# Kernel optimization log

Hardware: AMD Instinct MI355X
Metric: run time of the kernel (lower is better)

## Reference

```python
import jax, jax.numpy as jnp
import numpy as np

H = 1024
F = 4096  # base_ffn_dim = hidden * 4
WIDTHS = [256, 512]  # adapters; idx 2 -> width==hidden -> identity
EPS = 1e-5


def _xavier(key, fan_in, fan_out, gain):
    a = gain * np.sqrt(6.0 / (fan_in + fan_out))
    return jax.random.uniform(key, (fan_in, fan_out), jnp.float32, -a, a)


def _layernorm(x, g, b):
    mu = jnp.mean(x, axis=-1, keepdims=True)
    var = jnp.var(x, axis=-1, keepdims=True)
    return (x - mu) * jax.lax.rsqrt(var + EPS) * g + b


def setup_inputs() -> dict:
    key = jax.random.key(0)
    ks = jax.random.split(key, 12)
    g = 1.0 / np.sqrt(2.0)
    B, S = 4, 2048
    return {
        "x": jax.random.normal(ks[0], (B, S, H), jnp.float32),
        "width_multiplier": jax.random.uniform(ks[1], (B, S, 1), jnp.float32),
        "width_idx": jax.random.randint(ks[2], (B, S), 0, 3, jnp.int32),
        "ln_in_g": jnp.ones((H,), jnp.float32),
        "ln_in_b": jnp.zeros((H,), jnp.float32),
        "W1": _xavier(ks[3], H, F, g),
        "b1": jnp.zeros((F,), jnp.float32),
        "ln_h_g": jnp.ones((F,), jnp.float32),
        "ln_h_b": jnp.zeros((F,), jnp.float32),
        "W2": _xavier(ks[4], F, H, g),
        "b2": jnp.zeros((H,), jnp.float32),
        "a256_w1": _xavier(ks[5], H, 256, g),
        "a256_b1": jnp.zeros((256,), jnp.float32),
        "a256_w2": _xavier(ks[6], 256, H, g),
        "a256_b2": jnp.zeros((H,), jnp.float32),
        "a512_w1": _xavier(ks[7], H, 512, g),
        "a512_b1": jnp.zeros((512,), jnp.float32),
        "a512_w2": _xavier(ks[8], 512, H, g),
        "a512_b2": jnp.zeros((H,), jnp.float32),
    }


def reference(x, width_multiplier, width_idx,
              ln_in_g, ln_in_b, W1, b1, ln_h_g, ln_h_b, W2, b2,
              a256_w1, a256_b1, a256_w2, a256_b2,
              a512_w1, a512_b1, a512_w2, a512_b2):
    gelu = lambda t: jax.nn.gelu(t, approximate=False)  # torch nn.GELU exact
    x_norm = _layernorm(x, ln_in_g, ln_in_b)
    # base FFN path
    h = gelu(jnp.einsum("bsh,hf->bsf", x_norm, W1) + b1)
    h = _layernorm(h, ln_h_g, ln_h_b)
    base = jnp.einsum("bsf,fh->bsh", h, W2) + b2
    # width adapters (routed per token by width_idx)
    ad0 = jnp.einsum("bsw,wh->bsh", gelu(jnp.einsum("bsh,hw->bsw", x_norm, a256_w1) + a256_b1), a256_w2) + a256_b2
    ad1 = jnp.einsum("bsw,wh->bsh", gelu(jnp.einsum("bsh,hw->bsw", x_norm, a512_w1) + a512_b1), a512_w2) + a512_b2
    idx = width_idx[..., None]
    adaptive = jnp.where(idx == 0, ad0, jnp.where(idx == 1, ad1, x_norm))
    return base * width_multiplier + adaptive * (1.0 - width_multiplier)
```

## Files before the change

kernel.cpp:

```cpp
#include <hip/hip_runtime.h>
#include <cstdint>
#include <cstddef>

typedef unsigned short u16x8 __attribute__((ext_vector_type(8)));
typedef unsigned short u16x4 __attribute__((ext_vector_type(4)));
typedef __bf16 bf16x8 __attribute__((ext_vector_type(8)));
typedef float f32x4 __attribute__((ext_vector_type(4)));

__device__ __forceinline__ float b2f(unsigned short u) {
    union { unsigned int i; float f; } v;
    v.i = ((unsigned int)u) << 16;
    return v.f;
}

__device__ __forceinline__ unsigned short f2b(float f) {
    union { float f; unsigned int i; } v;
    v.f = f;
    unsigned int x = v.i;
    unsigned int lsb = (x >> 16) & 1u;
    x += 0x7FFFu + lsb;
    return (unsigned short)(x >> 16);
}

__device__ __forceinline__ float gelu_exact(float x) {
    return 0.5f * x * (1.0f + erff(x * 0.70710678118654752f));
}

__device__ __forceinline__ void ld_lds16(const unsigned short* g, unsigned short* l) {
    __builtin_amdgcn_global_load_lds(
        (const __attribute__((address_space(1))) void*)g,
        (__attribute__((address_space(3))) void*)l, 16, 0, 0);
}

__global__ void transpose_f32_bf16(const float* __restrict__ in,
                                   unsigned short* __restrict__ out, int R, int C,
                                   const float* __restrict__ scale) {
    __shared__ float tile[32][33];
    int x = blockIdx.x * 32 + threadIdx.x;
    int y0 = blockIdx.y * 32;
    for (int k = 0; k < 32; k += 8)
        tile[threadIdx.y + k][threadIdx.x] = in[(size_t)(y0 + threadIdx.y + k) * C + x];
    __syncthreads();
    int ox = y0 + threadIdx.x;
    int oy = blockIdx.x * 32;
    float sc = scale ? scale[ox] : 1.0f;
    for (int k = 0; k < 32; k += 8)
        out[(size_t)(oy + threadIdx.y + k) * R + ox] = f2b(tile[threadIdx.x][threadIdx.y + k] * sc);
}

__global__ void concat_bias(const float* __restrict__ b0, const float* __restrict__ b1,
                            float* __restrict__ out) {
    int t = threadIdx.x + blockIdx.x * blockDim.x;
    if (t < 256) out[t] = b0[t];
    else if (t < 768) out[t] = b1[t - 256];
}

__global__ void init_c01(const float* __restrict__ b2, float* __restrict__ c0b2,
                         float* __restrict__ c1) {
    int n = blockIdx.x * 256 + threadIdx.x;
    c0b2[n] = b2[n];
    c1[n] = 0.0f;
}

__global__ void prep_c01(const float* __restrict__ W2, const float* __restrict__ g,
                         const float* __restrict__ b, float* __restrict__ c0b2,
                         float* __restrict__ c1, int K, int N) {
    int n = blockIdx.x * 256 + threadIdx.x;
    int k0 = blockIdx.y * 256;
    float p0 = 0.f, p1 = 0.f;
    for (int k = k0; k < k0 + 256; ++k) {
        float w = W2[(size_t)k * N + n];
        p0 += b[k] * w;
        p1 += g[k] * w;
    }
    atomicAdd(&c0b2[n], p0);
    atomicAdd(&c1[n], p1);
}

__global__ __launch_bounds__(256) void rowstats4096(const unsigned short* __restrict__ h,
                                                    float* __restrict__ st) {
    const int row = blockIdx.x;
    const int t = threadIdx.x;
    const u16x8* p = (const u16x8*)(h + (size_t)row * 4096);
    float s = 0.f, s2 = 0.f;
#pragma unroll
    for (int i = 0; i < 2; ++i) {
        u16x8 v = p[t + (i << 8)];
#pragma unroll
        for (int r = 0; r < 8; ++r) { float f = b2f(v[r]); s += f; s2 += f * f; }
    }
#pragma unroll
    for (int o = 32; o > 0; o >>= 1) {
        s  += __shfl_down(s, o, 64);
        s2 += __shfl_down(s2, o, 64);
    }
    __shared__ float red[8];
    int lane = t & 63, w = t >> 6;
    if (lane == 0) { red[w] = s; red[4 + w] = s2; }
    __syncthreads();
    if (t == 0) {
        float ss = red[0] + red[1] + red[2] + red[3];
        float qq = red[4] + red[5] + red[6] + red[7];
        const float inv = 1.0f / 4096.0f;
        float mu = ss * inv;
        float var = qq * inv - mu * mu;
        float rs = rsqrtf(var + 1e-5f);
        st[2 * (size_t)row]     = rs;
        st[2 * (size_t)row + 1] = rs * mu;
    }
}

__global__ __launch_bounds__(256) void ln1024(const float* __restrict__ in,
                                              unsigned short* __restrict__ out,
                                              const float* __restrict__ g,
                                              const float* __restrict__ b) {
    const int row = blockIdx.x;
    const int t = threadIdx.x;
    f32x4 v = ((const f32x4*)(in + (size_t)row * 1024))[t];
    float s = v[0] + v[1] + v[2] + v[3];
    float s2 = v[0] * v[0] + v[1] * v[1] + v[2] * v[2] + v[3] * v[3];
#pragma unroll
    for (int o = 32; o > 0; o >>= 1) {
        s  += __shfl_down(s, o, 64);
        s2 += __shfl_down(s2, o, 64);
    }
    __shared__ float red[8];
    int lane = t & 63, w = t >> 6;
    if (lane == 0) { red[w] = s; red[4 + w] = s2; }
    __syncthreads();
    if (t == 0) {
        red[0] = red[0] + red[1] + red[2] + red[3];
        red[4] = red[4] + red[5] + red[6] + red[7];
    }
    __syncthreads();
    const float inv_n = 1.0f / 1024.0f;
    float mu = red[0] * inv_n;
    float var = red[4] * inv_n - mu * mu;
    float rs = rsqrtf(var + 1e-5f);
    f32x4 gv = ((const f32x4*)g)[t];
    f32x4 bv = ((const f32x4*)b)[t];
    u16x4 ov;
#pragma unroll
    for (int r = 0; r < 4; ++r) ov[r] = f2b((v[r] - mu) * rs * gv[r] + bv[r]);
    ((u16x4*)(out + (size_t)row * 1024))[t] = ov;
}

template <int EPI>
__global__ __launch_bounds__(256) void gemm_bt(
    const unsigned short* __restrict__ A, int lda,
    const unsigned short* __restrict__ BT, int ldb,
    const float* __restrict__ bias, unsigned short* __restrict__ Cb,
    float* __restrict__ Cf, int M, int N, int K,
    const int* __restrict__ idx, int match,
    const float* __restrict__ wm,
    const unsigned short* __restrict__ adaptive,
    const unsigned short* __restrict__ xn,
    const float* __restrict__ c1v,
    const float* __restrict__ rstat) {
    __shared__ __align__(16) unsigned short As[2][128 * 32];
    __shared__ __align__(16) unsigned short Bs[2][128 * 32];

    const int t = threadIdx.x;

    int id = blockIdx.y * gridDim.x + blockIdx.x;
    const int nwg = gridDim.x * gridDim.y;
    if ((nwg & 7) == 0) {
        const int cpx = nwg >> 3;
        id = (id & 7) * cpx + (id >> 3);
    }
    const int bx = id % gridDim.x;
    const int by = id / gridDim.x;
    const int m0 = by * 128;
    const int n0 = bx * 128;

    const int lane = t & 63;
    const int wid = t >> 6;

    const int srow = lane >> 2;
    const int sch  = (lane & 3) ^ (srow & 3);
    const int scol = sch << 3;

    const int wr = (wid >> 1) << 6;
    const int wc = (wid & 1) << 6;
    const int ml = lane & 15;
    const int q = lane >> 4;
    const int qsw = ((q ^ (ml & 3)) << 3);

    f32x4 acc[4][4];
#pragma unroll
    for (int i = 0; i < 4; ++i)
#pragma unroll
        for (int j = 0; j < 4; ++j)
#pragma unroll
            for (int r = 0; r < 4; ++r) acc[i][j][r] = 0.0f;

    const int nk = K >> 5;

#define STAGE(KT, BUF)                                                          \
    {                                                                           \
        _Pragma("unroll")                                                       \
        for (int hh = 0; hh < 2; ++hh) {                                        \
            int rbase = wid * 32 + hh * 16;                                     \
            int row = rbase + srow;                                             \
            ld_lds16(A  + (size_t)(m0 + row) * lda + (KT) * 32 + scol,          \
                     &As[BUF][rbase * 32]);                                     \
            ld_lds16(BT + (size_t)(n0 + row) * ldb + (KT) * 32 + scol,          \
                     &Bs[BUF][rbase * 32]);                                     \
        }                                                                       \
    }

    STAGE(0, 0);
    for (int kt = 0; kt < nk; ++kt) {
        const int cur = kt & 1;
        __syncthreads();
        if (kt + 1 < nk) STAGE(kt + 1, cur ^ 1);

        bf16x8 af[4], bf[4];
#pragma unroll
        for (int i = 0; i < 4; ++i)
            af[i] = *(const bf16x8*)(&As[cur][(wr + i * 16 + ml) * 32 + qsw]);
#pragma unroll
        for (int j = 0; j < 4; ++j)
            bf[j] = *(const bf16x8*)(&Bs[cur][(wc + j * 16 + ml) * 32 + qsw]);
#pragma unroll
        for (int i = 0; i < 4; ++i)
#pragma unroll
            for (int j = 0; j < 4; ++j)
                acc[i][j] = __builtin_amdgcn_mfma_f32_16x16x32_bf16(af[i], bf[j], acc[i][j], 0, 0, 0);
    }
#undef STAGE

#pragma unroll
    for (int i = 0; i < 4; ++i) {
        float rsv[4], rmv[4], wv[4];
        int idv[4];
        if (EPI == 1 || EPI == 2) {
#pragma unroll
            for (int r = 0; r < 4; ++r) {
                int row = m0 + wr + i * 16 + q * 4 + r;
                idv[r] = idx[row];
                if (EPI == 2) {
                    wv[r] = wm[row];
                    rsv[r] = rstat[2 * (size_t)row];
                    rmv[r] = rstat[2 * (size_t)row + 1];
                }
            }
        }
#pragma unroll
        for (int j = 0; j < 4; ++j) {
            int col = n0 + wc + j * 16 + ml;
            float bv = bias[col];
            float c1c = (EPI == 2) ? c1v[col] : 0.0f;
#pragma unroll
            for (int r = 0; r < 4; ++r) {
                int row = m0 + wr + i * 16 + q * 4 + r;
                size_t off = (size_t)row * N + col;
                if (EPI == 0) {
                    Cb[off] = f2b(gelu_exact(acc[i][j][r] + bv));
                } else if (EPI == 1) {
                    if (idv[r] == match) Cb[off] = f2b(acc[i][j][r] + bv);
                } else {
                    float bval = rsv[r] * acc[i][j][r] + bv - rmv[r] * c1c;
                    float a = b2f((idv[r] <= 1) ? adaptive[off] : xn[off]);
                    Cf[off] = bval * wv[r] + a * (1.0f - wv[r]);
                }
            }
        }
    }
}

extern "C" void kernel_launch(void* const* d_in, const int* in_sizes, int n_in,
                              void* d_out, int out_size, void* d_ws, size_t ws_size,
                              hipStream_t stream) {
    const float* x       = (const float*)d_in[0];
    const float* wm      = (const float*)d_in[1];
    const int*   widx    = (const int*)d_in[2];
    const float* ln_in_g = (const float*)d_in[3];
    const float* ln_in_b = (const float*)d_in[4];
    const float* W1      = (const float*)d_in[5];
    const float* b1      = (const float*)d_in[6];
    const float* ln_h_g  = (const float*)d_in[7];
    const float* ln_h_b  = (const float*)d_in[8];
    const float* W2      = (const float*)d_in[9];
    const float* b2      = (const float*)d_in[10];
    const float* a256_w1 = (const float*)d_in[11];
    const float* a256_b1 = (const float*)d_in[12];
    const float* a256_w2 = (const float*)d_in[13];
    const float* a256_b2 = (const float*)d_in[14];
    const float* a512_w1 = (const float*)d_in[15];
    const float* a512_b1 = (const float*)d_in[16];
    const float* a512_w2 = (const float*)d_in[17];
    const float* a512_b2 = (const float*)d_in[18];
    float* out = (float*)d_out;

    const int T = 8192, H = 1024, F = 4096;

    unsigned short* ws0   = (unsigned short*)d_ws;
    unsigned short* xn    = ws0;
    unsigned short* h     = xn    + (size_t)T * H;
    unsigned short* tt    = h     + (size_t)T * F;
    unsigned short* adp   = tt    + (size_t)T * 768;
    unsigned short* W1T   = adp   + (size_t)T * H;
    unsigned short* W2T   = W1T   + (size_t)H * F;
    unsigned short* awup  = W2T   + (size_t)F * H;
    unsigned short* aw2T0 = awup  + (size_t)768 * H;
    unsigned short* aw2T1 = aw2T0 + (size_t)H * 256;
    float*          ab1   = (float*)(aw2T1 + (size_t)H * 512);
    float*          stats = ab1 + 768;
    float*          c0b2  = stats + (size_t)T * 2;
    float*          c1    = c0b2 + H;

    dim3 tb(32, 8);
    init_c01<<<H / 256, 256, 0, stream>>>(b2, c0b2, c1);
    prep_c01<<<dim3(H / 256, F / 256), 256, 0, stream>>>(W2, ln_h_g, ln_h_b, c0b2, c1, F, H);

    transpose_f32_bf16<<<dim3(F / 32,   H / 32), tb, 0, stream>>>(W1, W1T, H, F, nullptr);
    transpose_f32_bf16<<<dim3(H / 32,   F / 32), tb, 0, stream>>>(W2, W2T, F, H, ln_h_g);
    transpose_f32_bf16<<<dim3(256 / 32, H / 32), tb, 0, stream>>>(a256_w1, awup, H, 256, nullptr);
    transpose_f32_bf16<<<dim3(512 / 32, H / 32), tb, 0, stream>>>(a512_w1, awup + (size_t)256 * H, H, 512, nullptr);
    transpose_f32_bf16<<<dim3(H / 32, 256 / 32), tb, 0, stream>>>(a256_w2, aw2T0, 256, H, nullptr);
    transpose_f32_bf16<<<dim3(H / 32, 512 / 32), tb, 0, stream>>>(a512_w2, aw2T1, 512, H, nullptr);
    concat_bias<<<3, 256, 0, stream>>>(a256_b1, a512_b1, ab1);

    ln1024<<<T, 256, 0, stream>>>(x, xn, ln_in_g, ln_in_b);

    gemm_bt<0><<<dim3(F / 128, T / 128), 256, 0, stream>>>(
        xn, H, W1T, H, b1, h, nullptr, T, F, H, nullptr, 0, nullptr, nullptr, nullptr, nullptr, nullptr);

    rowstats4096<<<T, 256, 0, stream>>>(h, stats);

    gemm_bt<0><<<dim3(768 / 128, T / 128), 256, 0, stream>>>(
        xn, H, awup, H, ab1, tt, nullptr, T, 768, H, nullptr, 0, nullptr, nullptr, nullptr, nullptr, nullptr);

    gemm_bt<1><<<dim3(H / 128, T / 128), 256, 0, stream>>>(
        tt, 768, aw2T0, 256, a256_b2, adp, nullptr, T, H, 256, widx, 0, nullptr, nullptr, nullptr, nullptr, nullptr);
    gemm_bt<1><<<dim3(H / 128, T / 128), 256, 0, stream>>>(
        tt + 256, 768, aw2T1, 512, a512_b2, adp, nullptr, T, H, 512, widx, 1, nullptr, nullptr, nullptr, nullptr, nullptr);

    gemm_bt<2><<<dim3(H / 128, T / 128), 256, 0, stream>>>(
        h, F, W2T, F, c0b2, nullptr, out, T, H, F, widx, 0, wm, adp, xn, c1, stats);
}
```

Measured before the change: 460.6 us.

## Add 256x256-tile 8-wave GEMM with grid swizzle for the W1 up-projection

Replaces the 128x128 generic GEMM used for the first FFN GEMM (8192x4096x1024) with a dedicated 256x256 tile kernel. It uses 512 threads, BK=64 double-buffered LDS loads, XOR-swizzled LDS layout, s_setprio around MFMA clusters and an XCD-aware block remap. The larger tile raises arithmetic intensity and cuts global traffic per FLOP. In exchange it uses 128KB of LDS per block, which limits occupancy, and the grid shrinks to 512 blocks, which risks wave-quantization tail effects across CUs.

```diff
diff --git a/kernel.cpp b/kernel.cpp
--- a/kernel.cpp
+++ b/kernel.cpp
@@ -143,6 +143,133 @@
 #pragma unroll
     for (int r = 0; r < 4; ++r) ov[r] = f2b((v[r] - mu) * rs * gv[r] + bv[r]);
     ((u16x4*)(out + (size_t)row * 1024))[t] = ov;
+}
+
+__global__ __launch_bounds__(512, 2) void gemm256_gelu(
+    const unsigned short* __restrict__ A, int lda,
+    const unsigned short* __restrict__ BT, int ldb,
+    const float* __restrict__ bias, unsigned short* __restrict__ Cb,
+    int M, int N, int K) {
+    __shared__ __align__(16) unsigned short As[2][256 * 64];
+    __shared__ __align__(16) unsigned short Bs[2][256 * 64];
+
+    const int t = threadIdx.x;
+
+    int id = blockIdx.y * gridDim.x + blockIdx.x;
+    const int nwg = gridDim.x * gridDim.y;
+    {
+        const int cpx = nwg >> 3;
+        id = (id & 7) * cpx + (id >> 3);
+    }
+    const int m0 = (id / gridDim.x) * 256;
+    const int n0 = (id % gridDim.x) * 256;
+
+    const int lane = t & 63;
+    const int wid = t >> 6;
+    const int wmr = (wid >> 2) << 7;
+    const int wnr = (wid & 3) << 6;
+    const int ml = lane & 15;
+    const int q = lane >> 4;
+
+    const int srow8 = lane >> 3;
+    const int scol = (((lane & 7) ^ (srow8 & 7)) << 3);
+
+    const int c0 = ((q ^ (ml & 7)) << 3);
+    const int c1 = c0 ^ 32;
+
+    f32x4 acc[8][4];
+#pragma unroll
+    for (int i = 0; i < 8; ++i)
+#pragma unroll
+        for (int j = 0; j < 4; ++j)
+#pragma unroll
+            for (int r = 0; r < 4; ++r) acc[i][j][r] = 0.0f;
+
+    const int nk = K >> 6;
+
+#define STAGE256(KT, BUF)                                                       \
+    {                                                                           \
+        const unsigned short* asrc =                                            \
+            A + (size_t)(m0 + wid * 8 + srow8) * lda + (KT) * 64 + scol;        \
+        const unsigned short* bsrc =                                            \
+            BT + (size_t)(n0 + wid * 8 + srow8) * ldb + (KT) * 64 + scol;       \
+        _Pragma("unroll")                                                       \
+        for (int s = 0; s < 4; ++s) {                                           \
+            ld_lds16(asrc + (size_t)s * 64 * lda, &As[BUF][(s * 64 + wid * 8) * 64]); \
+            ld_lds16(bsrc + (size_t)s * 64 * ldb, &Bs[BUF][(s * 64 + wid * 8) * 64]); \
+        }                                                                       \
+    }
+
+#define LDA256(QI)                                                              \
+    _Pragma("unroll")                                                           \
+    for (int i2 = 0; i2 < 4; ++i2) {                                            \
+        int row = wmr + (QI) * 64 + i2 * 16 + ml;                               \
+        afq[i2][0] = *(const bf16x8*)(&As[cur][(row << 6) + c0]);               \
+        afq[i2][1] = *(const bf16x8*)(&As[cur][(row << 6) + c1]);               \
+    }
+
+#define LDB256(DST, QJ)                                                         \
+    _Pragma("unroll")                                                           \
+    for (int j2 = 0; j2 < 2; ++j2) {                                            \
+        int row = wnr + (QJ) * 32 + j2 * 16 + ml;                               \
+        DST[j2][0] = *(const bf16x8*)(&Bs[cur][(row << 6) + c0]);               \
+        DST[j2][1] = *(const bf16x8*)(&Bs[cur][(row << 6) + c1]);               \
+    }
+
+#define MFMA16(I0, J0, BF)                                                      \
+    __builtin_amdgcn_s_barrier();                                               \
+    __builtin_amdgcn_s_setprio(1);                                              \
+    _Pragma("unroll")                                                           \
+    for (int i2 = 0; i2 < 4; ++i2)                                              \
+        _Pragma("unroll")                                                       \
+        for (int j2 = 0; j2 < 2; ++j2) {                                        \
+            acc[(I0) + i2][(J0) + j2] = __builtin_amdgcn_mfma_f32_16x16x32_bf16( \
+                afq[i2][0], BF[j2][0], acc[(I0) + i2][(J0) + j2], 0, 0, 0);     \
+            acc[(I0) + i2][(J0) + j2] = __builtin_amdgcn_mfma_f32_16x16x32_bf16( \
+                afq[i2][1], BF[j2][1], acc[(I0) + i2][(J0) + j2], 0, 0, 0);     \
+        }                                                                       \
+    __builtin_amdgcn_s_setprio(0);                                              \
+    __builtin_amdgcn_s_barrier();
+
+    STAGE256(0, 0);
+    for (int kt = 0; kt < nk; ++kt) {
+        const int cur = kt & 1;
+        if (kt + 1 < nk) {
+            STAGE256(kt + 1, cur ^ 1);
+            asm volatile("s_waitcnt vmcnt(8)" ::: "memory");
+        } else {
+            asm volatile("s_waitcnt vmcnt(0)" ::: "memory");
+        }
+        __builtin_amdgcn_s_barrier();
+
+        bf16x8 afq[4][2], b0f[2][2], b1f[2][2];
+        LDA256(0);
+        LDB256(b0f, 0);
+        MFMA16(0, 0, b0f);
+        LDB256(b1f, 1);
+        MFMA16(0, 2, b1f);
+        LDA256(1);
+        MFMA16(4, 2, b1f);
+        MFMA16(4, 0, b0f);
+    }
+#undef STAGE256
+#undef LDA256
+#undef LDB256
+#undef MFMA16
+
+#pragma unroll
+    for (int i = 0; i < 8; ++i) {
+#pragma unroll
+        for (int j = 0; j < 4; ++j) {
+            int col = n0 + wnr + j * 16 + ml;
+            float bv = bias[col];
+#pragma unroll
+            for (int r = 0; r < 4; ++r) {
+                int row = m0 + wmr + i * 16 + q * 4 + r;
+                Cb[(size_t)row * N + col] = f2b(gelu_exact(acc[i][j][r] + bv));
+            }
+        }
+    }
 }
 
 template <int EPI>
@@ -324,8 +451,8 @@
 
     ln1024<<<T, 256, 0, stream>>>(x, xn, ln_in_g, ln_in_b);
 
-    gemm_bt<0><<<dim3(F / 128, T / 128), 256, 0, stream>>>(
-        xn, H, W1T, H, b1, h, nullptr, T, F, H, nullptr, 0, nullptr, nullptr, nullptr, nullptr, nullptr);
+    gemm256_gelu<<<dim3(F / 256, T / 256), 512, 0, stream>>>(
+        xn, H, W1T, H, b1, h, T, F, H);
 
     rowstats4096<<<T, 256, 0, stream>>>(h, stats);
 
```

Result: slower. 471.5 us (+2.4%).

## Merge prep, adapter and stats kernels into fewer horizontally fused launches

Applied to the files above, without the earlier changes.

Combines all weight transposes, bias concat, the c0/c1 precompute and the input layernorm into one block-dispatched prep kernel. The adapter up-projection GEMM now shares a launch with the hidden row statistics, and the two adapter down-projection GEMMs share a single launch, cutting launch count and inter-kernel gaps so independent small work can overlap. The c01 precompute drops atomics in favour of 4 blocks each looping over the full K, which serialises that work into a long tail inside the prep kernel. Larger fused kernels may also have higher register and shared-memory footprints for the simple branches.

```diff
diff --git a/kernel.cpp b/kernel.cpp
--- a/kernel.cpp
+++ b/kernel.cpp
@@ -32,89 +32,50 @@
         (__attribute__((address_space(3))) void*)l, 16, 0, 0);
 }
 
-__global__ void transpose_f32_bf16(const float* __restrict__ in,
-                                   unsigned short* __restrict__ out, int R, int C,
-                                   const float* __restrict__ scale) {
+
+__device__ __forceinline__ void transp_body(const float* __restrict__ in,
+                                            unsigned short* __restrict__ out,
+                                            int R, int C,
+                                            const float* __restrict__ scale,
+                                            int bx, int by) {
     __shared__ float tile[32][33];
-    int x = blockIdx.x * 32 + threadIdx.x;
-    int y0 = blockIdx.y * 32;
+    const int tx = threadIdx.x & 31;
+    const int ty = threadIdx.x >> 5;
+    int x = bx * 32 + tx;
+    int y0 = by * 32;
     for (int k = 0; k < 32; k += 8)
-        tile[threadIdx.y + k][threadIdx.x] = in[(size_t)(y0 + threadIdx.y + k) * C + x];
+        tile[ty + k][tx] = in[(size_t)(y0 + ty + k) * C + x];
     __syncthreads();
-    int ox = y0 + threadIdx.x;
-    int oy = blockIdx.x * 32;
+    int ox = y0 + tx;
+    int oy = bx * 32;
     float sc = scale ? scale[ox] : 1.0f;
     for (int k = 0; k < 32; k += 8)
-        out[(size_t)(oy + threadIdx.y + k) * R + ox] = f2b(tile[threadIdx.x][threadIdx.y + k] * sc);
-}
-
-__global__ void concat_bias(const float* __restrict__ b0, const float* __restrict__ b1,
-                            float* __restrict__ out) {
-    int t = threadIdx.x + blockIdx.x * blockDim.x;
-    if (t < 256) out[t] = b0[t];
-    else if (t < 768) out[t] = b1[t - 256];
-}
-
-__global__ void init_c01(const float* __restrict__ b2, float* __restrict__ c0b2,
-                         float* __restrict__ c1) {
-    int n = blockIdx.x * 256 + threadIdx.x;
-    c0b2[n] = b2[n];
-    c1[n] = 0.0f;
-}
-
-__global__ void prep_c01(const float* __restrict__ W2, const float* __restrict__ g,
-                         const float* __restrict__ b, float* __restrict__ c0b2,
-                         float* __restrict__ c1, int K, int N) {
-    int n = blockIdx.x * 256 + threadIdx.x;
-    int k0 = blockIdx.y * 256;
+        out[(size_t)(oy + ty + k) * R + ox] = f2b(tile[tx][ty + k] * sc);
+}
+
+__device__ __forceinline__ void c01_body(const float* __restrict__ W2,
+                                         const float* __restrict__ g,
+                                         const float* __restrict__ b,
+                                         const float* __restrict__ b2,
+                                         float* __restrict__ c0b2,
+                                         float* __restrict__ c1,
+                                         int K, int N, int blocal) {
+    int n = (blocal << 8) + threadIdx.x;
     float p0 = 0.f, p1 = 0.f;
-    for (int k = k0; k < k0 + 256; ++k) {
+    for (int k = 0; k < K; ++k) {
         float w = W2[(size_t)k * N + n];
         p0 += b[k] * w;
         p1 += g[k] * w;
     }
-    atomicAdd(&c0b2[n], p0);
-    atomicAdd(&c1[n], p1);
-}
-
-__global__ __launch_bounds__(256) void rowstats4096(const unsigned short* __restrict__ h,
-                                                    float* __restrict__ st) {
-    const int row = blockIdx.x;
-    const int t = threadIdx.x;
-    const u16x8* p = (const u16x8*)(h + (size_t)row * 4096);
-    float s = 0.f, s2 = 0.f;
-#pragma unroll
-    for (int i = 0; i < 2; ++i) {
-        u16x8 v = p[t + (i << 8)];
-#pragma unroll
-        for (int r = 0; r < 8; ++r) { float f = b2f(v[r]); s += f; s2 += f * f; }
-    }
-#pragma unroll
-    for (int o = 32; o > 0; o >>= 1) {
-        s  += __shfl_down(s, o, 64);
-        s2 += __shfl_down(s2, o, 64);
-    }
-    __shared__ float red[8];
-    int lane = t & 63, w = t >> 6;
-    if (lane == 0) { red[w] = s; red[4 + w] = s2; }
-    __syncthreads();
-    if (t == 0) {
-        float ss = red[0] + red[1] + red[2] + red[3];
-        float qq = red[4] + red[5] + red[6] + red[7];
-        const float inv = 1.0f / 4096.0f;
-        float mu = ss * inv;
-        float var = qq * inv - mu * mu;
-        float rs = rsqrtf(var + 1e-5f);
-        st[2 * (size_t)row]     = rs;
-        st[2 * (size_t)row + 1] = rs * mu;
-    }
-}
-
-__global__ __launch_bounds__(256) void ln1024(const float* __restrict__ in,
-                                              unsigned short* __restrict__ out,
-                                              const float* __restrict__ g,
-                                              const float* __restrict__ b) {
-    const int row = blockIdx.x;
+    c0b2[n] = p0 + b2[n];
+    c1[n] = p1;
+}
+
+__device__ __forceinline__ void ln1024_body(const float* __restrict__ in,
+                                            unsigned short* __restrict__ out,
+                                            const float* __restrict__ g,
+                                            const float* __restrict__ b,
+                                            int row) {
     const int t = threadIdx.x;
     f32x4 v = ((const f32x4*)(in + (size_t)row * 1024))[t];
     float s = v[0] + v[1] + v[2] + v[3];
@@ -145,31 +106,62 @@
     ((u16x4*)(out + (size_t)row * 1024))[t] = ov;
 }
 
+__device__ __forceinline__ void rowstats_body(const unsigned short* __restrict__ h,
+                                              float* __restrict__ st, int row) {
+    const int t = threadIdx.x;
+    const u16x8* p = (const u16x8*)(h + (size_t)row * 4096);
+    float s = 0.f, s2 = 0.f;
+#pragma unroll
+    for (int i = 0; i < 2; ++i) {
+        u16x8 v = p[t + (i << 8)];
+#pragma unroll
+        for (int r = 0; r < 8; ++r) { float f = b2f(v[r]); s += f; s2 += f * f; }
+    }
+#pragma unroll
+    for (int o = 32; o > 0; o >>= 1) {
+        s  += __shfl_down(s, o, 64);
+        s2 += __shfl_down(s2, o, 64);
+    }
+    __shared__ float red2[8];
+    int lane = t & 63, w = t >> 6;
+    if (lane == 0) { red2[w] = s; red2[4 + w] = s2; }
+    __syncthreads();
+    if (t == 0) {
+        float ss = red2[0] + red2[1] + red2[2] + red2[3];
+        float qq = red2[4] + red2[5] + red2[6] + red2[7];
+        const float inv = 1.0f / 4096.0f;
+        float mu = ss * inv;
+        float var = qq * inv - mu * mu;
+        float rs = rsqrtf(var + 1e-5f);
+        st[2 * (size_t)row]     = rs;
+        st[2 * (size_t)row + 1] = rs * mu;
+    }
+}
+
 template <int EPI>
-__global__ __launch_bounds__(256) void gemm_bt(
+__device__ __forceinline__ void gemm_body(
+    unsigned short (*As)[128 * 32], unsigned short (*Bs)[128 * 32],
+    int fid, int nbx, int nby,
     const unsigned short* __restrict__ A, int lda,
     const unsigned short* __restrict__ BT, int ldb,
     const float* __restrict__ bias, unsigned short* __restrict__ Cb,
-    float* __restrict__ Cf, int M, int N, int K,
+    float* __restrict__ Cf, int N, int K,
     const int* __restrict__ idx, int match,
     const float* __restrict__ wm,
     const unsigned short* __restrict__ adaptive,
     const unsigned short* __restrict__ xn,
     const float* __restrict__ c1v,
     const float* __restrict__ rstat) {
-    __shared__ __align__(16) unsigned short As[2][128 * 32];
-    __shared__ __align__(16) unsigned short Bs[2][128 * 32];
-
     const int t = threadIdx.x;
 
-    int id = blockIdx.y * gridDim.x + blockIdx.x;
-    const int nwg = gridDim.x * gridDim.y;
+    int id = fid;
+    const int nwg = nbx * nby;
     if ((nwg & 7) == 0) {
         const int cpx = nwg >> 3;
         id = (id & 7) * cpx + (id >> 3);
     }
-    const int bx = id % gridDim.x;
-    const int by = id / gridDim.x;
+    const int bx = id % nbx;
+    const int by = id / nbx;
     const int m0 = by * 128;
     const int n0 = bx * 128;
 
@@ -266,6 +258,103 @@
                 }
             }
         }
+    }
+}
+
+__global__ __launch_bounds__(256) void mega_prep(
+    const float* __restrict__ W1, const float* __restrict__ W2,
+    const float* __restrict__ ln_h_g, const float* __restrict__ ln_h_b,
+    const float* __restrict__ a256_w1, const float* __restrict__ a512_w1,
+    const float* __restrict__ a256_w2, const float* __restrict__ a512_w2,
+    const float* __restrict__ a256_b1, const float* __restrict__ a512_b1,
+    const float* __restrict__ b2,
+    const float* __restrict__ x, const float* __restrict__ ln_in_g,
+    const float* __restrict__ ln_in_b,
+    unsigned short* __restrict__ W1T, unsigned short* __restrict__ W2T,
+    unsigned short* __restrict__ awup, unsigned short* __restrict__ aw2T0,
+    unsigned short* __restrict__ aw2T1, float* __restrict__ ab1,
+    float* __restrict__ c0b2, float* __restrict__ c1,
+    unsigned short* __restrict__ xn) {
+    const int H = 1024, F = 4096;
+    int bid = blockIdx.x;
+    if (bid < 4096) {
+        transp_body(W1, W1T, H, F, nullptr, bid & 127, bid >> 7);
+    } else if (bid < 8192) {
+        int l = bid - 4096;
+        transp_body(W2, W2T, F, H, ln_h_g, l & 31, l >> 5);
+    } else if (bid < 8448) {
+        int l = bid - 8192;
+        transp_body(a256_w1, awup, H, 256, nullptr, l & 7, l >> 3);
+    } else if (bid < 8960) {
+        int l = bid - 8448;
+        transp_body(a512_w1, awup + (size_t)256 * H, H, 512, nullptr, l & 15, l >> 4);
+    } else if (bid < 9216) {
+        int l = bid - 8960;
+        transp_body(a256_w2, aw2T0, 256, H, nullptr, l & 31, l >> 5);
+    } else if (bid < 9728) {
+        int l = bid - 9216;
+        transp_body(a512_w2, aw2T1, 512, H, nullptr, l & 31, l >> 5);
+    } else if (bid < 9731) {
+        int n = (bid - 9728) * 256 + threadIdx.x;
+        if (n < 768) ab1[n] = (n < 256) ? a256_b1[n] : a512_b1[n - 256];
+    } else if (bid < 9735) {
+        c01_body(W2, ln_h_g, ln_h_b, b2, c0b2, c1, F, H, bid - 9731);
+    } else {
+        ln1024_body(x, xn, ln_in_g, ln_in_b, bid - 9735);
+    }
+}
+
+template <int EPI>
+__global__ __launch_bounds__(256) void gemm_bt(
+    const unsigned short* __restrict__ A, int lda,
+    const unsigned short* __restrict__ BT, int ldb,
+    const float* __restrict__ bias, unsigned short* __restrict__ Cb,
+    float* __restrict__ Cf, int N, int K,
+    const int* __restrict__ idx, int match,
+    const float* __restrict__ wm,
+    const unsigned short* __restrict__ adaptive,
+    const unsigned short* __restrict__ xn,
+    const float* __restrict__ c1v,
+    const float* __restrict__ rstat) {
+    __shared__ __align__(16) unsigned short As[2][128 * 32];
+    __shared__ __align__(16) unsigned short Bs[2][128 * 32];
+    gemm_body<EPI>(As, Bs, blockIdx.y * gridDim.x + blockIdx.x,
+                   gridDim.x, gridDim.y, A, lda, BT, ldb, bias, Cb, Cf, N, K,
+                   idx, match, wm, adaptive, xn, c1v, rstat);
+}
+
+__global__ __launch_bounds__(256) void up_stats(
+    const unsigned short* __restrict__ xn, const unsigned short* __restrict__ awup,
+    const float* __restrict__ ab1, unsigned short* __restrict__ tt,
+    const unsigned short* __restrict__ h, float* __restrict__ st) {
+    __shared__ __align__(16) unsigned short As[2][128 * 32];
+    __shared__ __align__(16) unsigned short Bs[2][128 * 32];
+    int bid = blockIdx.x;
+    if (bid < 384) {
+        gemm_body<0>(As, Bs, bid, 6, 64, xn, 1024, awup, 1024, ab1, tt,
+                     nullptr, 768, 1024, nullptr, 0, nullptr, nullptr, nullptr,
+                     nullptr, nullptr);
+    } else {
+        rowstats_body(h, st, bid - 384);
+    }
+}
+
+__global__ __launch_bounds__(256) void downs(
+    const unsigned short* __restrict__ tt,
+    const unsigned short* __restrict__ aw2T0, const unsigned short* __restrict__ aw2T1,
+    const float* __restrict__ a256_b2, const float* __restrict__ a512_b2,
+    unsigned short* __restrict__ adp, const int* __restrict__ widx) {
+    __shared__ __align__(16) unsigned short As[2][128 * 32];
+    __shared__ __align__(16) unsigned short Bs[2][128 * 32];
+    int bid = blockIdx.x;
+    if (bid < 512) {
+        gemm_body<1>(As, Bs, bid, 8, 64, tt, 768, aw2T0, 256, a256_b2, adp,
+                     nullptr, 1024, 256, widx, 0, nullptr, nullptr, nullptr,
+                     nullptr, nullptr);
+    } else {
+        gemm_body<1>(As, Bs, bid - 512, 8, 64, tt + 256, 768, aw2T1, 512,
+                     a512_b2, adp, nullptr, 1024, 512, widx, 1, nullptr,
+                     nullptr, nullptr, nullptr, nullptr);
     }
 }
 
@@ -310,33 +399,19 @@
     float*          c0b2  = stats + (size_t)T * 2;
     float*          c1    = c0b2 + H;
 
-    dim3 tb(32, 8);
-    init_c01<<<H / 256, 256, 0, stream>>>(b2, c0b2, c1);
-    prep_c01<<<dim3(H / 256, F / 256), 256, 0, stream>>>(W2, ln_h_g, ln_h_b, c0b2, c1, F, H);
-
-    transpose_f32_bf16<<<dim3(F / 32,   H / 32), tb, 0, stream>>>(W1, W1T, H, F, nullptr);
-    transpose_f32_bf16<<<dim3(H / 32,   F / 32), tb, 0, stream>>>(W2, W2T, F, H, ln_h_g);
-    transpose_f32_bf16<<<dim3(256 / 32, H / 32), tb, 0, stream>>>(a256_w1, awup, H, 256, nullptr);
-    transpose_f32_bf16<<<dim3(512 / 32, H / 32), tb, 0, stream>>>(a512_w1, awup + (size_t)256 * H, H, 512, nullptr);
-    transpose_f32_bf16<<<dim3(H / 32, 256 / 32), tb, 0, stream>>>(a256_w2, aw2T0, 256, H, nullptr);
-    transpose_f32_bf16<<<dim3(H / 32, 512 / 32), tb, 0, stream>>>(a512_w2, aw2T1, 512, H, nullptr);
-    concat_bias<<<3, 256, 0, stream>>>(a256_b1, a512_b1, ab1);
-
-    ln1024<<<T, 256, 0, stream>>>(x, xn, ln_in_g, ln_in_b);
+    mega_prep<<<9735 + T, 256, 0, stream>>>(
+        W1, W2, ln_h_g, ln_h_b, a256_w1, a512_w1, a256_w2, a512_w2,
+        a256_b1, a512_b1, b2, x, ln_in_g, ln_in_b,
+        W1T, W2T, awup, aw2T0, aw2T1, ab1, c0b2, c1, xn);
 
     gemm_bt<0><<<dim3(F / 128, T / 128), 256, 0, stream>>>(
-        xn, H, W1T, H, b1, h, nullptr, T, F, H, nullptr, 0, nullptr, nullptr, nullptr, nullptr, nullptr);
-
-    rowstats4096<<<T, 256, 0, stream>>>(h, stats);
-
-    gemm_bt<0><<<dim3(768 / 128, T / 128), 256, 0, stream>>>(
-        xn, H, awup, H, ab1, tt, nullptr, T, 768, H, nullptr, 0, nullptr, nullptr, nullptr, nullptr, nullptr);
-
-    gemm_bt<1><<<dim3(H / 128, T / 128), 256, 0, stream>>>(
-        tt, 768, aw2T0, 256, a256_b2, adp, nullptr, T, H, 256, widx, 0, nullptr, nullptr, nullptr, nullptr, nullptr);
-    gemm_bt<1><<<dim3(H / 128, T / 128), 256, 0, stream>>>(
-        tt + 256, 768, aw2T1, 512, a512_b2, adp, nullptr, T, H, 512, widx, 1, nullptr, nullptr, nullptr, nullptr, nullptr);
+        xn, H, W1T, H, b1, h, nullptr, F, H, nullptr, 0, nullptr, nullptr,
+        nullptr, nullptr, nullptr);
+
+    up_stats<<<384 + T, 256, 0, stream>>>(xn, awup, ab1, tt, h, stats);
+
+    downs<<<1024, 256, 0, stream>>>(tt, aw2T0, aw2T1, a256_b2, a512_b2, adp, widx);
 
     gemm_bt<2><<<dim3(H / 128, T / 128), 256, 0, stream>>>(
-        h, F, W2T, F, c0b2, nullptr, out, T, H, F, widx, 0, wm, adp, xn, c1, stats);
-}
+        h, F, W2T, F, c0b2, nullptr, out, H, F, widx, 0, wm, adp, xn, c1, stats);
+}
```

New measurement: 599.1 us. 30.1% more time.
